# Optimization experiments

Hardware: AMD Instinct MI355X
Metric: run time of the kernel (lower is better)

The kernel has to match this reference:

```python
import jax, jax.numpy as jnp
import numpy as np

N = 50000        # nodes
E = 800000       # edges (before self-loops)
F_IN = 128       # input node features
HID = 64         # GAT hidden per head
HEADS1 = 4
NUM_GRAPHS = 64
NEG_SLOPE = 0.2  # PyG GATConv default leaky_relu slope


def setup_inputs() -> dict:
    key = jax.random.key(0)
    ks = jax.random.split(key, 12)
    x = jax.random.normal(ks[0], (N, F_IN), dtype=jnp.float32)
    edge_index = jax.random.randint(ks[1], (2, E), 0, N, dtype=jnp.int32)
    batch = jnp.sort(jax.random.randint(ks[2], (N,), 0, NUM_GRAPHS, dtype=jnp.int32))
    s = 1.0 / np.sqrt(F_IN)
    W1 = jax.random.uniform(ks[3], (F_IN, HEADS1 * HID), jnp.float32, -s, s)
    att_src1 = jax.random.uniform(ks[4], (HEADS1, HID), jnp.float32, -s, s)
    att_dst1 = jax.random.uniform(ks[5], (HEADS1, HID), jnp.float32, -s, s)
    b1 = jnp.zeros((HEADS1 * HID,), jnp.float32)
    s2 = 1.0 / np.sqrt(HEADS1 * HID)
    W2 = jax.random.uniform(ks[6], (HEADS1 * HID, HID), jnp.float32, -s2, s2)
    att_src2 = jax.random.uniform(ks[7], (1, HID), jnp.float32, -s2, s2)
    att_dst2 = jax.random.uniform(ks[8], (1, HID), jnp.float32, -s2, s2)
    b2 = jnp.zeros((HID,), jnp.float32)
    return {"x": x, "edge_index": edge_index, "batch": batch,
            "W1": W1, "att_src1": att_src1, "att_dst1": att_dst1, "b1": b1,
            "W2": W2, "att_src2": att_src2, "att_dst2": att_dst2, "b2": b2}


def gat_conv(x, src, dst, W, a_src, a_dst, bias, heads, out_dim):
    # PyG GATConv: h = x @ W (no lin bias); per-node attention logits;
    # e_ij = leaky_relu(alpha_src[j] + alpha_dst[i]); softmax over dst groups;
    # out_i = sum_j alpha_ij * h_j; concat heads; + bias.
    n = x.shape[0]
    h = (x @ W).reshape(n, heads, out_dim)                 # [N,H,C]
    alpha_src = jnp.einsum('nhc,hc->nh', h, a_src)         # [N,H]
    alpha_dst = jnp.einsum('nhc,hc->nh', h, a_dst)         # [N,H]
    e = jax.nn.leaky_relu(alpha_src[src] + alpha_dst[dst], NEG_SLOPE)  # [E,H]
    m = jax.ops.segment_max(e, dst, num_segments=n)        # segment softmax (stable)
    e = jnp.exp(e - m[dst])
    denom = jax.ops.segment_sum(e, dst, num_segments=n)
    alpha = e / denom[dst]                                 # [E,H]
    msg = h[src] * alpha[:, :, None]                       # [E,H,C]
    agg = jax.ops.segment_sum(msg, dst, num_segments=n)    # [N,H,C]
    return agg.reshape(n, heads * out_dim) + bias


def reference(x, edge_index, batch, W1, att_src1, att_dst1, b1, W2, att_src2, att_dst2, b2):
    # add self loops (PyG GATConv default add_self_loops=True)
    loops = jnp.arange(N, dtype=edge_index.dtype)
    src = jnp.concatenate([edge_index[0], loops])
    dst = jnp.concatenate([edge_index[1], loops])
    h = jax.nn.relu(gat_conv(x, src, dst, W1, att_src1, att_dst1, b1, HEADS1, HID))
    h = gat_conv(h, src, dst, W2, att_src2, att_dst2, b2, 1, HID)
    # global mean pool over graphs
    sums = jax.ops.segment_sum(h, batch, num_segments=NUM_GRAPHS)
    cnt = jax.ops.segment_sum(jnp.ones((N,), h.dtype), batch, num_segments=NUM_GRAPHS)
    return sums / jnp.maximum(cnt, 1.0)[:, None]
```

## Files before the change

kernel.cpp:

```cpp
#include <hip/hip_runtime.h>
#include <math.h>


typedef unsigned short ushort_t;
typedef __bf16 bf16x8 __attribute__((ext_vector_type(8)));
typedef float  f32x4  __attribute__((ext_vector_type(4)));

__device__ inline float bf2f(ushort_t u) { return __uint_as_float((unsigned)u << 16); }
__device__ inline ushort_t f2bf(float x) {
  unsigned b = __float_as_uint(x);
  return (ushort_t)((b + 0x7fff + ((b >> 16) & 1)) >> 16);
}
__device__ inline float leaky(float v) { return (v > 0.f) ? v : 0.2f * v; }

__device__ inline f32x4 mfma16(bf16x8 a, bf16x8 b, f32x4 c) {
  return __builtin_amdgcn_mfma_f32_16x16x32_bf16(a, b, c, 0, 0, 0);
}

__global__ void k_hist(const int* __restrict__ edst, int E, int N, int* __restrict__ deg) {
  int stride = gridDim.x * blockDim.x;
  int EE = E + N;
  for (int i = blockIdx.x * blockDim.x + threadIdx.x; i < EE; i += stride) {
    int d = (i < E) ? edst[i] : (i - E);
    atomicAdd(&deg[d], 1);
  }
}

__global__ void k_gbounds_zero(const int* __restrict__ batch, int N, int G,
                               int* __restrict__ gstart, int* __restrict__ deg) {
  int stride = gridDim.x * blockDim.x;
  for (int i = blockIdx.x * blockDim.x + threadIdx.x; i < N; i += stride) {
    deg[i] = 0;
    int b = batch[i];
    int bp = (i == 0) ? -1 : batch[i - 1];
    for (int g = bp + 1; g <= b; ++g) gstart[g] = i;
    if (i == N - 1)
      for (int g = b + 1; g <= G; ++g) gstart[g] = N;
  }
}

__global__ void k_scan_bsum(const int* __restrict__ deg, int n, int* __restrict__ bsum) {
  __shared__ int ws[16];
  int tid = threadIdx.x, lane = tid & 63, wv = tid >> 6;
  int i = blockIdx.x * 1024 + tid;
  int v = (i < n) ? deg[i] : 0;
  #pragma unroll
  for (int off = 1; off < 64; off <<= 1) v += __shfl_xor(v, off);
  if (lane == 0) ws[wv] = v;
  __syncthreads();
  if (tid < 16) {
    int s = ws[tid];
    #pragma unroll
    for (int off = 1; off < 16; off <<= 1) s += __shfl_xor(s, off);
    if (tid == 0) bsum[blockIdx.x] = s;
  }
}

__global__ void k_scan_bbase(const int* __restrict__ bsum, int nb,
                             int* __restrict__ bbase, int* __restrict__ offsets, int n) {
  int lane = threadIdx.x & 63;
  int v = (lane < nb) ? bsum[lane] : 0;
  int x = v;
  #pragma unroll
  for (int off = 1; off < 64; off <<= 1) {
    int t = __shfl_up(x, off);
    if (lane >= off) x += t;
  }
  if (lane < nb) bbase[lane] = x - v;
  if (lane == nb - 1) offsets[n] = x;
}

__global__ void k_scan_final(const int* __restrict__ deg, int n,
                             const int* __restrict__ bbase,
                             int* __restrict__ offsets, int* __restrict__ cursor) {
  __shared__ int wsum[16];
  int tid = threadIdx.x, lane = tid & 63, wv = tid >> 6;
  int i = blockIdx.x * 1024 + tid;
  int v = (i < n) ? deg[i] : 0;
  int x = v;
  #pragma unroll
  for (int off = 1; off < 64; off <<= 1) {
    int t = __shfl_up(x, off);
    if (lane >= off) x += t;
  }
  if (lane == 63) wsum[wv] = x;
  __syncthreads();
  if (wv == 0 && lane < 16) {
    int s = wsum[lane];
    #pragma unroll
    for (int off = 1; off < 16; off <<= 1) {
      int t = __shfl_up(s, off);
      if (lane >= off) s += t;
    }
    wsum[lane] = s;
  }
  __syncthreads();
  int wbase = (wv == 0) ? 0 : wsum[wv - 1];
  int incl = bbase[blockIdx.x] + wbase + x;
  if (i < n) { int o = incl - v; offsets[i] = o; cursor[i] = o; }
}

__global__ void k_scatter(const int* __restrict__ esrc, const int* __restrict__ edst,
                          int E, int N, int* __restrict__ cursor,
                          int2* __restrict__ sed) {
  int stride = gridDim.x * blockDim.x;
  int EE = E + N;
  for (int i = blockIdx.x * blockDim.x + threadIdx.x; i < EE; i += stride) {
    int d, s;
    if (i < E) { d = edst[i]; s = esrc[i]; }
    else       { d = i - E;   s = i - E;   }
    int pos = atomicAdd(&cursor[d], 1);
    sed[pos] = make_int2(s, d);
  }
}

__device__ inline void packB_one(const float* __restrict__ B, ushort_t* __restrict__ bh,
                                 ushort_t* __restrict__ bl, int K, int Nn, int t) {
  int KT = K >> 5;
  int l = t & 63, fb = t >> 6;
  int nt = fb / KT, kt = fb - nt * KT;
  int col = nt * 16 + (l & 15);
  int k0 = kt * 32 + (l >> 4) * 8;
  ushort_t h[8], lo[8];
  #pragma unroll
  for (int j = 0; j < 8; ++j) {
    float v = B[(size_t)(k0 + j) * Nn + col];
    h[j] = f2bf(v);
    lo[j] = f2bf(v - bf2f(h[j]));
  }
  size_t o = (size_t)t * 8;
  *(ushort4*)(bh + o)     = make_ushort4(h[0], h[1], h[2], h[3]);
  *(ushort4*)(bh + o + 4) = make_ushort4(h[4], h[5], h[6], h[7]);
  *(ushort4*)(bl + o)     = make_ushort4(lo[0], lo[1], lo[2], lo[3]);
  *(ushort4*)(bl + o + 4) = make_ushort4(lo[4], lo[5], lo[6], lo[7]);
}

__global__ void k_packB_all(const float* __restrict__ W1, const float* __restrict__ W2,
                            ushort_t* __restrict__ B1h, ushort_t* __restrict__ B1l,
                            ushort_t* __restrict__ B2h, ushort_t* __restrict__ B2l) {
  int t = blockIdx.x * blockDim.x + threadIdx.x;
  if (t < 4096) packB_one(W1, B1h, B1l, 128, 256, t);
  else if (t < 6144) packB_one(W2, B2h, B2l, 256, 64, t - 4096);
}

template<int KT, int TERMS, int WM>
__global__ __launch_bounds__(256)
void k_gemm_att(const float* __restrict__ Af32, const ushort_t* __restrict__ Ah,
                const ushort_t* __restrict__ Bh, const ushort_t* __restrict__ Bl,
                const float* __restrict__ a_srcW, const float* __restrict__ a_dstW,
                ushort_t* __restrict__ hb, float* __restrict__ as_,
                float* __restrict__ ad_, int M, int Nn, int H) {
  const int tid = threadIdx.x;
  const int w = tid >> 6, lane = tid & 63;
  const int wm = w & (WM - 1), wn = w / WM;
  const int m0w = blockIdx.x * (WM * 32) + wm * 32;
  const int n0  = blockIdx.y * ((4 / WM) * 64) + wn * 64;
  const int head = n0 >> 6;
  const int mt0 = m0w >> 4, nt0 = n0 >> 4;

  const float* pX[2];
  int rowmi[2];
  const ushort_t* pAh[2];
  #pragma unroll
  for (int mi = 0; mi < 2; ++mi) {
    if constexpr (TERMS == 3) {
      rowmi[mi] = (mt0 + mi) * 16 + (lane & 15);
      pX[mi] = Af32 + (size_t)rowmi[mi] * (KT * 32) + ((lane >> 4) << 3);
    } else {
      size_t fa = (size_t)(mt0 + mi) * KT;
      pAh[mi] = Ah + fa * 512 + (size_t)lane * 8;
    }
  }
  const ushort_t* pBh[4];
  const ushort_t* pBl[4];
  #pragma unroll
  for (int ni = 0; ni < 4; ++ni) {
    size_t fb = (size_t)(nt0 + ni) * KT;
    pBh[ni] = Bh + fb * 512 + (size_t)lane * 8;
    pBl[ni] = Bl + fb * 512 + (size_t)lane * 8;
  }

  f32x4 acc[2][4];
  #pragma unroll
  for (int mi = 0; mi < 2; ++mi)
    #pragma unroll
    for (int ni = 0; ni < 4; ++ni)
      acc[mi][ni] = (f32x4){0.f, 0.f, 0.f, 0.f};

  for (int kt = 0; kt < KT; ++kt) {
    const size_t ko = (size_t)kt * 512;
    bf16x8 ahf[2], alf[2], bhf[4], blf[4];
    #pragma unroll
    for (int mi = 0; mi < 2; ++mi) {
      if constexpr (TERMS == 3) {
        float v[8] = {0.f, 0.f, 0.f, 0.f, 0.f, 0.f, 0.f, 0.f};
        if (rowmi[mi] < M) {
          float4 a = *(const float4*)(pX[mi] + kt * 32);
          float4 b = *(const float4*)(pX[mi] + kt * 32 + 4);
          v[0] = a.x; v[1] = a.y; v[2] = a.z; v[3] = a.w;
          v[4] = b.x; v[5] = b.y; v[6] = b.z; v[7] = b.w;
        }
        union { ushort_t u[8]; bf16x8 f; } uh, ul;
        #pragma unroll
        for (int j = 0; j < 8; ++j) {
          uh.u[j] = f2bf(v[j]);
          ul.u[j] = f2bf(v[j] - bf2f(uh.u[j]));
        }
        ahf[mi] = uh.f;
        alf[mi] = ul.f;
      } else {
        ahf[mi] = *(const bf16x8*)(pAh[mi] + ko);
      }
    }
    #pragma unroll
    for (int ni = 0; ni < 4; ++ni) {
      bhf[ni] = *(const bf16x8*)(pBh[ni] + ko);
      blf[ni] = *(const bf16x8*)(pBl[ni] + ko);
    }
    #pragma unroll
    for (int mi = 0; mi < 2; ++mi)
      #pragma unroll
      for (int ni = 0; ni < 4; ++ni) {
        if constexpr (TERMS == 3)
          acc[mi][ni] = mfma16(alf[mi], bhf[ni], acc[mi][ni]);
        acc[mi][ni] = mfma16(ahf[mi], blf[ni], acc[mi][ni]);
        acc[mi][ni] = mfma16(ahf[mi], bhf[ni], acc[mi][ni]);
      }
  }

  const int c16 = lane & 15, q = lane >> 4;
  float sv[4], dv[4];
  #pragma unroll
  for (int ni = 0; ni < 4; ++ni) {
    sv[ni] = a_srcW[head * 64 + ni * 16 + c16];
    dv[ni] = a_dstW[head * 64 + ni * 16 + c16];
  }
  #pragma unroll
  for (int mi = 0; mi < 2; ++mi) {
    #pragma unroll
    for (int r = 0; r < 4; ++r) {
      int gr = m0w + mi * 16 + q * 4 + r;
      float ps = acc[mi][0][r] * sv[0] + acc[mi][1][r] * sv[1] +
                 acc[mi][2][r] * sv[2] + acc[mi][3][r] * sv[3];
      float pd = acc[mi][0][r] * dv[0] + acc[mi][1][r] * dv[1] +
                 acc[mi][2][r] * dv[2] + acc[mi][3][r] * dv[3];
      #pragma unroll
      for (int off = 1; off < 16; off <<= 1) {
        ps += __shfl_xor(ps, off);
        pd += __shfl_xor(pd, off);
      }
      if (gr < M) {
        #pragma unroll
        for (int ni = 0; ni < 4; ++ni)
          hb[(size_t)gr * Nn + n0 + ni * 16 + c16] = f2bf(acc[mi][ni][r]);
        if (c16 == 0) { as_[gr * H + head] = ps; ad_[gr * H + head] = pd; }
      }
    }
  }
}

__global__ void k_edgew1(const int2* __restrict__ sed, const float* __restrict__ as1,
                         const float* __restrict__ ad1, float* __restrict__ w1, int EE) {
  int t = blockIdx.x * blockDim.x + threadIdx.x;
  if (t >= EE * 4) return;
  int e = t >> 2, h = t & 3;
  int2 p = sed[e];
  w1[t] = __expf(leaky(as1[p.x * 4 + h] + ad1[p.y * 4 + h]));
}

__global__ void k_edgew2(const int2* __restrict__ sed, const float* __restrict__ as2,
                         const float* __restrict__ ad2, float* __restrict__ w2, int EE) {
  int e = blockIdx.x * blockDim.x + threadIdx.x;
  if (e >= EE) return;
  int2 p = sed[e];
  w2[e] = __expf(leaky(as2[p.x] + ad2[p.y]));
}

__global__ void k_agg1(const ushort_t* __restrict__ h1b, const float* __restrict__ w1,
                       const int* __restrict__ offs, const int2* __restrict__ sed,
                       const float* __restrict__ b1, ushort_t* __restrict__ a2h, int N) {
  int gt = blockIdx.x * blockDim.x + threadIdx.x;
  int wid = gt >> 6, lane = gt & 63;
  if (wid >= N) return;
  int head = lane >> 4, sub = lane & 15, coff = sub << 2;
  int start = offs[wid], end = offs[wid + 1];

  float denom = 0.f;
  float4 acc = make_float4(0.f, 0.f, 0.f, 0.f);
  int e = start;
  for (; e + 8 <= end; e += 8) {
    int s0 = sed[e].x, s1 = sed[e + 1].x, s2 = sed[e + 2].x, s3 = sed[e + 3].x;
    int s4 = sed[e + 4].x, s5 = sed[e + 5].x, s6 = sed[e + 6].x, s7 = sed[e + 7].x;
    float wa = w1[(e + 0) * 4 + head], wb = w1[(e + 1) * 4 + head];
    float wc = w1[(e + 2) * 4 + head], wd = w1[(e + 3) * 4 + head];
    float we = w1[(e + 4) * 4 + head], wf = w1[(e + 5) * 4 + head];
    float wg = w1[(e + 6) * 4 + head], wh = w1[(e + 7) * 4 + head];
    ushort4 g0 = *(const ushort4*)(h1b + (size_t)s0 * 256 + head * 64 + coff);
    ushort4 g1 = *(const ushort4*)(h1b + (size_t)s1 * 256 + head * 64 + coff);
    ushort4 g2 = *(const ushort4*)(h1b + (size_t)s2 * 256 + head * 64 + coff);
    ushort4 g3 = *(const ushort4*)(h1b + (size_t)s3 * 256 + head * 64 + coff);
    ushort4 g4 = *(const ushort4*)(h1b + (size_t)s4 * 256 + head * 64 + coff);
    ushort4 g5 = *(const ushort4*)(h1b + (size_t)s5 * 256 + head * 64 + coff);
    ushort4 g6 = *(const ushort4*)(h1b + (size_t)s6 * 256 + head * 64 + coff);
    ushort4 g7 = *(const ushort4*)(h1b + (size_t)s7 * 256 + head * 64 + coff);
    denom += ((wa + wb) + (wc + wd)) + ((we + wf) + (wg + wh));
    acc.x += wa * bf2f(g0.x) + wb * bf2f(g1.x) + wc * bf2f(g2.x) + wd * bf2f(g3.x)
           + we * bf2f(g4.x) + wf * bf2f(g5.x) + wg * bf2f(g6.x) + wh * bf2f(g7.x);
    acc.y += wa * bf2f(g0.y) + wb * bf2f(g1.y) + wc * bf2f(g2.y) + wd * bf2f(g3.y)
           + we * bf2f(g4.y) + wf * bf2f(g5.y) + wg * bf2f(g6.y) + wh * bf2f(g7.y);
    acc.z += wa * bf2f(g0.z) + wb * bf2f(g1.z) + wc * bf2f(g2.z) + wd * bf2f(g3.z)
           + we * bf2f(g4.z) + wf * bf2f(g5.z) + wg * bf2f(g6.z) + wh * bf2f(g7.z);
    acc.w += wa * bf2f(g0.w) + wb * bf2f(g1.w) + wc * bf2f(g2.w) + wd * bf2f(g3.w)
           + we * bf2f(g4.w) + wf * bf2f(g5.w) + wg * bf2f(g6.w) + wh * bf2f(g7.w);
  }
  for (; e + 4 <= end; e += 4) {
    int s0 = sed[e].x, s1 = sed[e + 1].x, s2 = sed[e + 2].x, s3 = sed[e + 3].x;
    float wa = w1[(e + 0) * 4 + head], wb = w1[(e + 1) * 4 + head];
    float wc = w1[(e + 2) * 4 + head], wd = w1[(e + 3) * 4 + head];
    ushort4 g0 = *(const ushort4*)(h1b + (size_t)s0 * 256 + head * 64 + coff);
    ushort4 g1 = *(const ushort4*)(h1b + (size_t)s1 * 256 + head * 64 + coff);
    ushort4 g2 = *(const ushort4*)(h1b + (size_t)s2 * 256 + head * 64 + coff);
    ushort4 g3 = *(const ushort4*)(h1b + (size_t)s3 * 256 + head * 64 + coff);
    denom += (wa + wb) + (wc + wd);
    acc.x += wa * bf2f(g0.x) + wb * bf2f(g1.x) + wc * bf2f(g2.x) + wd * bf2f(g3.x);
    acc.y += wa * bf2f(g0.y) + wb * bf2f(g1.y) + wc * bf2f(g2.y) + wd * bf2f(g3.y);
    acc.z += wa * bf2f(g0.z) + wb * bf2f(g1.z) + wc * bf2f(g2.z) + wd * bf2f(g3.z);
    acc.w += wa * bf2f(g0.w) + wb * bf2f(g1.w) + wc * bf2f(g2.w) + wd * bf2f(g3.w);
  }
  for (; e < end; ++e) {
    int s = sed[e].x;
    float w = w1[e * 4 + head];
    ushort4 g = *(const ushort4*)(h1b + (size_t)s * 256 + head * 64 + coff);
    denom += w;
    acc.x += w * bf2f(g.x); acc.y += w * bf2f(g.y);
    acc.z += w * bf2f(g.z); acc.w += w * bf2f(g.w);
  }
  float inv = 1.f / denom;
  float4 bv = *(const float4*)(b1 + head * 64 + coff);
  int c0 = head * 64 + coff;
  int fa = (wid >> 4) * 8 + (c0 >> 5);
  int fl = (wid & 15) | (((c0 >> 3) & 3) << 4);
  size_t addr = ((size_t)fa * 64 + fl) * 8 + (c0 & 7);
  ushort4 o;
  o.x = f2bf(fmaxf(acc.x * inv + bv.x, 0.f));
  o.y = f2bf(fmaxf(acc.y * inv + bv.y, 0.f));
  o.z = f2bf(fmaxf(acc.z * inv + bv.z, 0.f));
  o.w = f2bf(fmaxf(acc.w * inv + bv.w, 0.f));
  *(ushort4*)(a2h + addr) = o;
}

__global__ void k_agg2(const ushort_t* __restrict__ h2b, const float* __restrict__ w2,
                       const int* __restrict__ offs, const int2* __restrict__ sed,
                       const float* __restrict__ b2, float* __restrict__ hfin, int N) {
  int gt = blockIdx.x * blockDim.x + threadIdx.x;
  int wid = gt >> 6, lane = gt & 63;
  if (wid >= N) return;
  int half = lane >> 5, li = lane & 31;
  int start = offs[wid], end = offs[wid + 1];

  float dn = 0.f, acc0 = 0.f, acc1 = 0.f;
  int e = start;
  for (; e + 8 <= end; e += 8) {
    int e0 = e + half, e1 = e + 2 + half, e2 = e + 4 + half, e3 = e + 6 + half;
    int s0 = sed[e0].x, s1 = sed[e1].x, s2 = sed[e2].x, s3 = sed[e3].x;
    float wa = w2[e0], wb = w2[e1], wc = w2[e2], wd = w2[e3];
    unsigned g0 = *(const unsigned*)(h2b + (size_t)s0 * 64 + li * 2);
    unsigned g1 = *(const unsigned*)(h2b + (size_t)s1 * 64 + li * 2);
    unsigned g2 = *(const unsigned*)(h2b + (size_t)s2 * 64 + li * 2);
    unsigned g3 = *(const unsigned*)(h2b + (size_t)s3 * 64 + li * 2);
    dn += (wa + wb) + (wc + wd);
    acc0 += wa * __uint_as_float(g0 << 16) + wb * __uint_as_float(g1 << 16)
          + wc * __uint_as_float(g2 << 16) + wd * __uint_as_float(g3 << 16);
    acc1 += wa * __uint_as_float(g0 & 0xffff0000u) + wb * __uint_as_float(g1 & 0xffff0000u)
          + wc * __uint_as_float(g2 & 0xffff0000u) + wd * __uint_as_float(g3 & 0xffff0000u);
  }
  for (; e + 2 <= end; e += 2) {
    int e0 = e + half;
    int s0 = sed[e0].x;
    float wa = w2[e0];
    unsigned g0 = *(const unsigned*)(h2b + (size_t)s0 * 64 + li * 2);
    dn += wa;
    acc0 += wa * __uint_as_float(g0 << 16);
    acc1 += wa * __uint_as_float(g0 & 0xffff0000u);
  }
  if (e < end && half == 0) {
    int s0 = sed[e].x;
    float wa = w2[e];
    unsigned g0 = *(const unsigned*)(h2b + (size_t)s0 * 64 + li * 2);
    dn += wa;
    acc0 += wa * __uint_as_float(g0 << 16);
    acc1 += wa * __uint_as_float(g0 & 0xffff0000u);
  }
  acc0 += __shfl_xor(acc0, 32);
  acc1 += __shfl_xor(acc1, 32);
  dn   += __shfl_xor(dn, 32);
  if (half == 0) {
    float inv = 1.f / dn;
    float2 bv = *(const float2*)(b2 + li * 2);
    float2 o;
    o.x = acc0 * inv + bv.x;
    o.y = acc1 * inv + bv.y;
    *(float2*)(hfin + (size_t)wid * 64 + li * 2) = o;
  }
}

__global__ void k_pool(const float* __restrict__ hfin, const int* __restrict__ gstart,
                       float* __restrict__ out) {
  int g = blockIdx.x;
  int c = threadIdx.x & 63, r = threadIdx.x >> 6;
  int start = gstart[g], cnt = gstart[g + 1] - start;
  float acc = 0.f;
  for (int i = r; i < cnt; i += 4)
    acc += hfin[(size_t)(start + i) * 64 + c];
  __shared__ float red[256];
  red[threadIdx.x] = acc;
  __syncthreads();
  if (r == 0)
    out[g * 64 + c] = (red[c] + red[64 + c] + red[128 + c] + red[192 + c]) /
                      fmaxf((float)cnt, 1.f);
}

extern "C" void kernel_launch(void* const* d_in, const int* in_sizes, int n_in,
                              void* d_out, int out_size, void* d_ws, size_t ws_size,
                              hipStream_t stream) {
  const float* x        = (const float*)d_in[0];
  const int*   ei       = (const int*)d_in[1];
  const int*   batch    = (const int*)d_in[2];
  const float* W1       = (const float*)d_in[3];
  const float* att_src1 = (const float*)d_in[4];
  const float* att_dst1 = (const float*)d_in[5];
  const float* b1       = (const float*)d_in[6];
  const float* W2       = (const float*)d_in[7];
  const float* att_src2 = (const float*)d_in[8];
  const float* att_dst2 = (const float*)d_in[9];
  const float* b2       = (const float*)d_in[10];
  float* out = (float*)d_out;

  const int N = in_sizes[0] / 128;
  const int E = in_sizes[1] / 2;
  const int EE = E + N;
  const int* esrc = ei;
  const int* edst = ei + E;

  const int GB2 = (N + 127) / 128;
  const int GB1 = GB2 * 2;
  const int MF  = GB2 * 8;
  const int NB  = (N + 1023) / 1024;

  char* p = (char*)d_ws;
  auto alloc = [&](size_t bytes) -> void* {
    void* r = (void*)p;
    p += (bytes + 255) & ~(size_t)255;
    return r;
  };
  ushort_t* A2h  = (ushort_t*)alloc((size_t)MF * 8 * 64 * 16);
  ushort_t* B1h  = (ushort_t*)alloc((size_t)16 * 4 * 64 * 16);
  ushort_t* B1l  = (ushort_t*)alloc((size_t)16 * 4 * 64 * 16);
  ushort_t* B2h  = (ushort_t*)alloc((size_t)4 * 8 * 64 * 16);
  ushort_t* B2l  = (ushort_t*)alloc((size_t)4 * 8 * 64 * 16);
  ushort_t* h1b  = (ushort_t*)alloc((size_t)N * 256 * 2);
  ushort_t* h2b  = (ushort_t*)alloc((size_t)N * 64 * 2);
  float*    hfin = (float*)alloc((size_t)N * 64 * 4);
  float*    as1  = (float*)alloc((size_t)N * 4 * 4);
  float*    ad1  = (float*)alloc((size_t)N * 4 * 4);
  float*    as2  = (float*)alloc((size_t)N * 4);
  float*    ad2  = (float*)alloc((size_t)N * 4);
  float*    w1   = (float*)alloc((size_t)EE * 4 * 4);
  float*    w2   = (float*)alloc((size_t)EE * 4);
  int*  deg     = (int*)alloc((size_t)N * 4);
  int*  offsets = (int*)alloc((size_t)(N + 1) * 4);
  int*  cursor  = (int*)alloc((size_t)N * 4);
  int2* sed     = (int2*)alloc((size_t)EE * 8);
  int*  bsum    = (int*)alloc(64 * 4);
  int*  bbase   = (int*)alloc(64 * 4);
  int*  gstart  = (int*)alloc(65 * 4);

  k_gbounds_zero<<<256, 256, 0, stream>>>(batch, N, 64, gstart, deg);
  k_hist<<<1024, 256, 0, stream>>>(edst, E, N, deg);
  k_scan_bsum<<<NB, 1024, 0, stream>>>(deg, N, bsum);
  k_scan_bbase<<<1, 64, 0, stream>>>(bsum, NB, bbase, offsets, N);
  k_scan_final<<<NB, 1024, 0, stream>>>(deg, N, bbase, offsets, cursor);
  k_scatter<<<1024, 256, 0, stream>>>(esrc, edst, E, N, cursor, sed);

  k_packB_all<<<24, 256, 0, stream>>>(W1, W2, B1h, B1l, B2h, B2l);

  k_gemm_att<4, 3, 2><<<dim3(GB1, 2), 256, 0, stream>>>(
      x, nullptr, B1h, B1l, att_src1, att_dst1, h1b, as1, ad1, N, 256, 4);
  k_edgew1<<<(EE * 4 + 255) / 256, 256, 0, stream>>>(sed, as1, ad1, w1, EE);
  int wave_blocks = (N * 64 + 255) / 256;
  k_agg1<<<wave_blocks, 256, 0, stream>>>(h1b, w1, offsets, sed, b1, A2h, N);

  k_gemm_att<8, 2, 4><<<dim3(GB2, 1), 256, 0, stream>>>(
      nullptr, A2h, B2h, B2l, att_src2, att_dst2, h2b, as2, ad2, N, 64, 1);
  k_edgew2<<<(EE + 255) / 256, 256, 0, stream>>>(sed, as2, ad2, w2, EE);
  k_agg2<<<wave_blocks, 256, 0, stream>>>(h2b, w2, offsets, sed, b2, hfin, N);

  k_pool<<<64, 256, 0, stream>>>(hfin, gstart, out);
}
```

Before: 308.9 us.

## Merge preprocessing kernels and co-schedule edge scatter with first GEMM

Histogram, graph-bounds and weight packing now run as block ranges of a single setup kernel, and the zeroing of the degree array moves to a memset. Self-loop degrees are added analytically in the scan instead of through atomics. The CSR scatter and the layer-1 GEMM share one launch via block-index dispatch, so independent work can overlap and launch count drops. This gives up per-kernel grid tuning (one thread per element instead of grid-stride loops) and mixes heterogeneous blocks in one launch.

```diff
diff --git a/kernel.cpp b/kernel.cpp
--- a/kernel.cpp
+++ b/kernel.cpp
@@ -15,103 +15,6 @@
 
 __device__ inline f32x4 mfma16(bf16x8 a, bf16x8 b, f32x4 c) {
   return __builtin_amdgcn_mfma_f32_16x16x32_bf16(a, b, c, 0, 0, 0);
-}
-
-__global__ void k_hist(const int* __restrict__ edst, int E, int N, int* __restrict__ deg) {
-  int stride = gridDim.x * blockDim.x;
-  int EE = E + N;
-  for (int i = blockIdx.x * blockDim.x + threadIdx.x; i < EE; i += stride) {
-    int d = (i < E) ? edst[i] : (i - E);
-    atomicAdd(&deg[d], 1);
-  }
-}
-
-__global__ void k_gbounds_zero(const int* __restrict__ batch, int N, int G,
-                               int* __restrict__ gstart, int* __restrict__ deg) {
-  int stride = gridDim.x * blockDim.x;
-  for (int i = blockIdx.x * blockDim.x + threadIdx.x; i < N; i += stride) {
-    deg[i] = 0;
-    int b = batch[i];
-    int bp = (i == 0) ? -1 : batch[i - 1];
-    for (int g = bp + 1; g <= b; ++g) gstart[g] = i;
-    if (i == N - 1)
-      for (int g = b + 1; g <= G; ++g) gstart[g] = N;
-  }
-}
-
-__global__ void k_scan_bsum(const int* __restrict__ deg, int n, int* __restrict__ bsum) {
-  __shared__ int ws[16];
-  int tid = threadIdx.x, lane = tid & 63, wv = tid >> 6;
-  int i = blockIdx.x * 1024 + tid;
-  int v = (i < n) ? deg[i] : 0;
-  #pragma unroll
-  for (int off = 1; off < 64; off <<= 1) v += __shfl_xor(v, off);
-  if (lane == 0) ws[wv] = v;
-  __syncthreads();
-  if (tid < 16) {
-    int s = ws[tid];
-    #pragma unroll
-    for (int off = 1; off < 16; off <<= 1) s += __shfl_xor(s, off);
-    if (tid == 0) bsum[blockIdx.x] = s;
-  }
-}
-
-__global__ void k_scan_bbase(const int* __restrict__ bsum, int nb,
-                             int* __restrict__ bbase, int* __restrict__ offsets, int n) {
-  int lane = threadIdx.x & 63;
-  int v = (lane < nb) ? bsum[lane] : 0;
-  int x = v;
-  #pragma unroll
-  for (int off = 1; off < 64; off <<= 1) {
-    int t = __shfl_up(x, off);
-    if (lane >= off) x += t;
-  }
-  if (lane < nb) bbase[lane] = x - v;
-  if (lane == nb - 1) offsets[n] = x;
-}
-
-__global__ void k_scan_final(const int* __restrict__ deg, int n,
-                             const int* __restrict__ bbase,
-                             int* __restrict__ offsets, int* __restrict__ cursor) {
-  __shared__ int wsum[16];
-  int tid = threadIdx.x, lane = tid & 63, wv = tid >> 6;
-  int i = blockIdx.x * 1024 + tid;
-  int v = (i < n) ? deg[i] : 0;
-  int x = v;
-  #pragma unroll
-  for (int off = 1; off < 64; off <<= 1) {
-    int t = __shfl_up(x, off);
-    if (lane >= off) x += t;
-  }
-  if (lane == 63) wsum[wv] = x;
-  __syncthreads();
-  if (wv == 0 && lane < 16) {
-    int s = wsum[lane];
-    #pragma unroll
-    for (int off = 1; off < 16; off <<= 1) {
-      int t = __shfl_up(s, off);
-      if (lane >= off) s += t;
-    }
-    wsum[lane] = s;
-  }
-  __syncthreads();
-  int wbase = (wv == 0) ? 0 : wsum[wv - 1];
-  int incl = bbase[blockIdx.x] + wbase + x;
-  if (i < n) { int o = incl - v; offsets[i] = o; cursor[i] = o; }
-}
-
-__global__ void k_scatter(const int* __restrict__ esrc, const int* __restrict__ edst,
-                          int E, int N, int* __restrict__ cursor,
-                          int2* __restrict__ sed) {
-  int stride = gridDim.x * blockDim.x;
-  int EE = E + N;
-  for (int i = blockIdx.x * blockDim.x + threadIdx.x; i < EE; i += stride) {
-    int d, s;
-    if (i < E) { d = edst[i]; s = esrc[i]; }
-    else       { d = i - E;   s = i - E;   }
-    int pos = atomicAdd(&cursor[d], 1);
-    sed[pos] = make_int2(s, d);
-  }
 }
 
 __device__ inline void packB_one(const float* __restrict__ B, ushort_t* __restrict__ bh,
@@ -135,26 +38,106 @@
   *(ushort4*)(bl + o + 4) = make_ushort4(lo[4], lo[5], lo[6], lo[7]);
 }
 
-__global__ void k_packB_all(const float* __restrict__ W1, const float* __restrict__ W2,
-                            ushort_t* __restrict__ B1h, ushort_t* __restrict__ B1l,
-                            ushort_t* __restrict__ B2h, ushort_t* __restrict__ B2l) {
-  int t = blockIdx.x * blockDim.x + threadIdx.x;
-  if (t < 4096) packB_one(W1, B1h, B1l, 128, 256, t);
-  else if (t < 6144) packB_one(W2, B2h, B2l, 256, 64, t - 4096);
+__global__ void k_setup(const int* __restrict__ edst, int E, int* __restrict__ deg,
+                        const int* __restrict__ batch, int N, int G,
+                        int* __restrict__ gstart,
+                        const float* __restrict__ W1, const float* __restrict__ W2,
+                        ushort_t* __restrict__ B1h, ushort_t* __restrict__ B1l,
+                        ushort_t* __restrict__ B2h, ushort_t* __restrict__ B2l,
+                        int HB, int GBB) {
+  int b = blockIdx.x, tid = threadIdx.x;
+  if (b < HB) {
+    int i = b * 256 + tid;
+    if (i < E) atomicAdd(&deg[edst[i]], 1);
+  } else if (b < HB + GBB) {
+    int i = (b - HB) * 256 + tid;
+    if (i < N) {
+      int bb = batch[i];
+      int bp = (i == 0) ? -1 : batch[i - 1];
+      for (int g = bp + 1; g <= bb; ++g) gstart[g] = i;
+      if (i == N - 1)
+        for (int g = bb + 1; g <= G; ++g) gstart[g] = N;
+    }
+  } else {
+    int t = (b - HB - GBB) * 256 + tid;
+    if (t < 4096) packB_one(W1, B1h, B1l, 128, 256, t);
+    else if (t < 6144) packB_one(W2, B2h, B2l, 256, 64, t - 4096);
+  }
+}
+
+__global__ void k_scan_bsum(const int* __restrict__ deg, int n, int* __restrict__ bsum) {
+  __shared__ int ws[16];
+  int tid = threadIdx.x, lane = tid & 63, wv = tid >> 6;
+  int i = blockIdx.x * 1024 + tid;
+  int v = (i < n) ? deg[i] + 1 : 0;
+  #pragma unroll
+  for (int off = 1; off < 64; off <<= 1) v += __shfl_xor(v, off);
+  if (lane == 0) ws[wv] = v;
+  __syncthreads();
+  if (tid < 16) {
+    int s = ws[tid];
+    #pragma unroll
+    for (int off = 1; off < 16; off <<= 1) s += __shfl_xor(s, off);
+    if (tid == 0) bsum[blockIdx.x] = s;
+  }
+}
+
+__global__ void k_scan_bbase(const int* __restrict__ bsum, int nb,
+                             int* __restrict__ bbase, int* __restrict__ offsets, int n) {
+  int lane = threadIdx.x & 63;
+  int v = (lane < nb) ? bsum[lane] : 0;
+  int x = v;
+  #pragma unroll
+  for (int off = 1; off < 64; off <<= 1) {
+    int t = __shfl_up(x, off);
+    if (lane >= off) x += t;
+  }
+  if (lane < nb) bbase[lane] = x - v;
+  if (lane == nb - 1) offsets[n] = x;
+}
+
+__global__ void k_scan_final(const int* __restrict__ deg, int n,
+                             const int* __restrict__ bbase,
+                             int* __restrict__ offsets, int* __restrict__ cursor) {
+  __shared__ int wsum[16];
+  int tid = threadIdx.x, lane = tid & 63, wv = tid >> 6;
+  int i = blockIdx.x * 1024 + tid;
+  int v = (i < n) ? deg[i] + 1 : 0;
+  int x = v;
+  #pragma unroll
+  for (int off = 1; off < 64; off <<= 1) {
+    int t = __shfl_up(x, off);
+    if (lane >= off) x += t;
+  }
+  if (lane == 63) wsum[wv] = x;
+  __syncthreads();
+  if (wv == 0 && lane < 16) {
+    int s = wsum[lane];
+    #pragma unroll
+    for (int off = 1; off < 16; off <<= 1) {
+      int t = __shfl_up(s, off);
+      if (lane >= off) s += t;
+    }
+    wsum[lane] = s;
+  }
+  __syncthreads();
+  int wbase = (wv == 0) ? 0 : wsum[wv - 1];
+  int incl = bbase[blockIdx.x] + wbase + x;
+  if (i < n) { int o = incl - v; offsets[i] = o; cursor[i] = o; }
 }
 
 template<int KT, int TERMS, int WM>
-__global__ __launch_bounds__(256)
-void k_gemm_att(const float* __restrict__ Af32, const ushort_t* __restrict__ Ah,
-                const ushort_t* __restrict__ Bh, const ushort_t* __restrict__ Bl,
-                const float* __restrict__ a_srcW, const float* __restrict__ a_dstW,
-                ushort_t* __restrict__ hb, float* __restrict__ as_,
-                float* __restrict__ ad_, int M, int Nn, int H) {
+__device__ void gemm_att_body(int bx, int by,
+                              const float* __restrict__ Af32, const ushort_t* __restrict__ Ah,
+                              const ushort_t* __restrict__ Bh, const ushort_t* __restrict__ Bl,
+                              const float* __restrict__ a_srcW, const float* __restrict__ a_dstW,
+                              ushort_t* __restrict__ hb, float* __restrict__ as_,
+                              float* __restrict__ ad_, int M, int Nn, int H) {
   const int tid = threadIdx.x;
   const int w = tid >> 6, lane = tid & 63;
   const int wm = w & (WM - 1), wn = w / WM;
-  const int m0w = blockIdx.x * (WM * 32) + wm * 32;
-  const int n0  = blockIdx.y * ((4 / WM) * 64) + wn * 64;
+  const int m0w = bx * (WM * 32) + wm * 32;
+  const int n0  = by * ((4 / WM) * 64) + wn * 64;
   const int head = n0 >> 6;
   const int mt0 = m0w >> 4, nt0 = n0 >> 4;
 
@@ -257,6 +240,42 @@
       }
     }
   }
+}
+
+__global__ __launch_bounds__(256)
+void k_scatter_gemm1(const int* __restrict__ esrc, const int* __restrict__ edst,
+                     int E, int N, int* __restrict__ cursor, int2* __restrict__ sed,
+                     int SCB,
+                     const float* __restrict__ x,
+                     const ushort_t* __restrict__ B1h, const ushort_t* __restrict__ B1l,
+                     const float* __restrict__ as_w, const float* __restrict__ ad_w,
+                     ushort_t* __restrict__ h1b, float* __restrict__ as1,
+                     float* __restrict__ ad1, int GB1) {
+  if (blockIdx.x < SCB) {
+    int i = blockIdx.x * 256 + threadIdx.x;
+    int EE = E + N;
+    if (i < EE) {
+      int d, s;
+      if (i < E) { d = edst[i]; s = esrc[i]; }
+      else       { d = i - E;   s = i - E;   }
+      int pos = atomicAdd(&cursor[d], 1);
+      sed[pos] = make_int2(s, d);
+    }
+  } else {
+    int b = blockIdx.x - SCB;
+    gemm_att_body<4, 3, 2>(b % GB1, b / GB1, x, nullptr, B1h, B1l,
+                           as_w, ad_w, h1b, as1, ad1, N, 256, 4);
+  }
+}
+
+__global__ __launch_bounds__(256)
+void k_gemm2(const ushort_t* __restrict__ A2h,
+             const ushort_t* __restrict__ B2h, const ushort_t* __restrict__ B2l,
+             const float* __restrict__ as_w, const float* __restrict__ ad_w,
+             ushort_t* __restrict__ h2b, float* __restrict__ as2,
+             float* __restrict__ ad2, int M) {
+  gemm_att_body<8, 2, 4>(blockIdx.x, 0, nullptr, A2h, B2h, B2l,
+                         as_w, ad_w, h2b, as2, ad2, M, 64, 1);
 }
 
 __global__ void k_edgew1(const int2* __restrict__ sed, const float* __restrict__ as1,
@@ -446,6 +465,9 @@
   const int GB1 = GB2 * 2;
   const int MF  = GB2 * 8;
   const int NB  = (N + 1023) / 1024;
+  const int HB  = (E + 255) / 256;
+  const int GBB = (N + 255) / 256;
+  const int SCB = (EE + 255) / 256;
 
   char* p = (char*)d_ws;
   auto alloc = [&](size_t bytes) -> void* {
@@ -475,23 +497,25 @@
   int*  bbase   = (int*)alloc(64 * 4);
   int*  gstart  = (int*)alloc(65 * 4);
 
-  k_gbounds_zero<<<256, 256, 0, stream>>>(batch, N, 64, gstart, deg);
-  k_hist<<<1024, 256, 0, stream>>>(edst, E, N, deg);
+  hipMemsetAsync(deg, 0, (size_t)N * 4, stream);
+
+  k_setup<<<HB + GBB + 24, 256, 0, stream>>>(edst, E, deg, batch, N, 64, gstart,
+                                             W1, W2, B1h, B1l, B2h, B2l, HB, GBB);
+
   k_scan_bsum<<<NB, 1024, 0, stream>>>(deg, N, bsum);
   k_scan_bbase<<<1, 64, 0, stream>>>(bsum, NB, bbase, offsets, N);
   k_scan_final<<<NB, 1024, 0, stream>>>(deg, N, bbase, offsets, cursor);
-  k_scatter<<<1024, 256, 0, stream>>>(esrc, edst, E, N, cursor, sed);
-
-  k_packB_all<<<24, 256, 0, stream>>>(W1, W2, B1h, B1l, B2h, B2l);
-
-  k_gemm_att<4, 3, 2><<<dim3(GB1, 2), 256, 0, stream>>>(
-      x, nullptr, B1h, B1l, att_src1, att_dst1, h1b, as1, ad1, N, 256, 4);
+
+  k_scatter_gemm1<<<SCB + GB1 * 2, 256, 0, stream>>>(
+      esrc, edst, E, N, cursor, sed, SCB,
+      x, B1h, B1l, att_src1, att_dst1, h1b, as1, ad1, GB1);
+
   k_edgew1<<<(EE * 4 + 255) / 256, 256, 0, stream>>>(sed, as1, ad1, w1, EE);
   int wave_blocks = (N * 64 + 255) / 256;
   k_agg1<<<wave_blocks, 256, 0, stream>>>(h1b, w1, offsets, sed, b1, A2h, N);
 
-  k_gemm_att<8, 2, 4><<<dim3(GB2, 1), 256, 0, stream>>>(
-      nullptr, A2h, B2h, B2l, att_src2, att_dst2, h2b, as2, ad2, N, 64, 1);
+  k_gemm2<<<GB2, 256, 0, stream>>>(A2h, B2h, B2l, att_src2, att_dst2,
+                                   h2b, as2, ad2, N);
   k_edgew2<<<(EE + 255) / 256, 256, 0, stream>>>(sed, as2, ad2, w2, EE);
   k_agg2<<<wave_blocks, 256, 0, stream>>>(h2b, w2, offsets, sed, b2, hfin, N);
 
```

Measured after the change: 317.1 us. 2.7% more time.
